# Kernel tuning notes

Hardware: AMD Instinct MI355X
Metric: run time of the kernel (lower is better)

The kernel has to match this reference:

```python
import jax, jax.numpy as jnp
import numpy as np

M, N = 4096, 4096

def _make_expk(n):
    k = np.arange(n, dtype=np.float64) * np.pi / (2.0 * n)
    return jnp.asarray(np.stack([np.cos(k), np.sin(k)], axis=-1), dtype=jnp.float32)

def setup_inputs() -> dict:
    key = jax.random.key(0)
    x = jax.random.normal(key, (M, N), dtype=jnp.float32)
    return {"x": x, "expkM": _make_expk(M), "expkN": _make_expk(N)}

def _idct_last(X, expk):
    """1D IDCT (inverse of unnormalized DCT-II) along last axis via Makhoul's
    N-point FFT trick. expk[k] = (cos, sin) of pi*k/(2N), i.e. e^{j pi k/(2N)}."""
    n = X.shape[-1]
    Xv = X * 0.5
    # V[k] = (Xv[k] - j*Xv[n-k]) * e^{j pi k/(2n)}, with imag part 0 at k=0
    tail = -jnp.flip(Xv, axis=-1)[..., :-1]
    Vi = jnp.concatenate([jnp.zeros_like(Xv[..., :1]), tail], axis=-1)
    W = expk[:, 0] + 1j * expk[:, 1]
    V = (Xv + 1j * Vi) * W
    v = jnp.fft.ifft(V, axis=-1).real.astype(X.dtype)
    # de-interleave: out[2m] = v[m], out[2m+1] = v[n-1-m]
    out = jnp.zeros_like(X)
    out = out.at[..., 0::2].set(v[..., : n - n // 2])
    out = out.at[..., 1::2].set(jnp.flip(v, axis=-1)[..., : n // 2])
    return out

def reference(x, expkM, expkN):
    # separable 2D IDCT: last axis (N) then first axis (M)
    y = _idct_last(x, expkN)
    y = _idct_last(y.T, expkM).T
    return y
```

## Files before the change

### kernel.cpp

```cpp
#include <hip/hip_runtime.h>
#include <math.h>


#define TT 256

constexpr float W64R[32] = {
    1.0f, 0.995184726672197f, 0.980785280403230f, 0.956940335732209f,
    0.923879532511287f, 0.881921264348355f, 0.831469612302545f, 0.773010453362737f,
    0.707106781186548f, 0.634393284163645f, 0.555570233019602f, 0.471396736825998f,
    0.382683432365090f, 0.290284677254462f, 0.195090322016128f, 0.0980171403295606f,
    0.0f, -0.0980171403295606f, -0.195090322016128f, -0.290284677254462f,
    -0.382683432365090f, -0.471396736825998f, -0.555570233019602f, -0.634393284163645f,
    -0.707106781186548f, -0.773010453362737f, -0.831469612302545f, -0.881921264348355f,
    -0.923879532511287f, -0.956940335732209f, -0.980785280403230f, -0.995184726672197f};
constexpr float W64I[32] = {
    0.0f, 0.0980171403295606f, 0.195090322016128f, 0.290284677254462f,
    0.382683432365090f, 0.471396736825998f, 0.555570233019602f, 0.634393284163645f,
    0.707106781186548f, 0.773010453362737f, 0.831469612302545f, 0.881921264348355f,
    0.923879532511287f, 0.956940335732209f, 0.980785280403230f, 0.995184726672197f,
    1.0f, 0.995184726672197f, 0.980785280403230f, 0.956940335732209f,
    0.923879532511287f, 0.881921264348355f, 0.831469612302545f, 0.773010453362737f,
    0.707106781186548f, 0.634393284163645f, 0.555570233019602f, 0.471396736825998f,
    0.382683432365090f, 0.290284677254462f, 0.195090322016128f, 0.0980171403295606f};

__device__ __forceinline__ constexpr int brev(int x, int bits) {
    int r = 0;
    for (int i = 0; i < bits; ++i) { r = (r << 1) | (x & 1); x >>= 1; }
    return r;
}

template <int NP>
__device__ __forceinline__ void fft_dif(float* re, float* im) {
#pragma unroll
    for (int h = NP / 2; h >= 1; h >>= 1) {
#pragma unroll
        for (int b = 0; b < NP; b += 2 * h) {
#pragma unroll
            for (int k = 0; k < h; ++k) {
                float ur = re[b + k], ui = im[b + k];
                float vr = re[b + k + h], vi = im[b + k + h];
                float dr = ur - vr, di = ui - vi;
                re[b + k] = ur + vr;
                im[b + k] = ui + vi;
                float wr = W64R[k * (32 / h)], wi = W64I[k * (32 / h)];
                re[b + k + h] = dr * wr - di * wi;
                im[b + k + h] = dr * wi + di * wr;
            }
        }
    }
}

#define C_SQ2 0.70710678118654752440f
__device__ __forceinline__ void radix8(const float* ar, const float* ai,
                                       float* tr, float* ti) {
    float s04r = ar[0] + ar[4], s04i = ai[0] + ai[4];
    float d04r = ar[0] - ar[4], d04i = ai[0] - ai[4];
    float s26r = ar[2] + ar[6], s26i = ai[2] + ai[6];
    float d26r = ar[2] - ar[6], d26i = ai[2] - ai[6];
    float E0r = s04r + s26r, E0i = s04i + s26i;
    float E1r = d04r - d26i, E1i = d04i + d26r;
    float E2r = s04r - s26r, E2i = s04i - s26i;
    float E3r = d04r + d26i, E3i = d04i - d26r;
    float s15r = ar[1] + ar[5], s15i = ai[1] + ai[5];
    float d15r = ar[1] - ar[5], d15i = ai[1] - ai[5];
    float s37r = ar[3] + ar[7], s37i = ai[3] + ai[7];
    float d37r = ar[3] - ar[7], d37i = ai[3] - ai[7];
    float O0r = s15r + s37r, O0i = s15i + s37i;
    float O1r = d15r - d37i, O1i = d15i + d37r;
    float O2r = s15r - s37r, O2i = s15i - s37i;
    float O3r = d15r + d37i, O3i = d15i - d37r;
    float W1r = C_SQ2 * (O1r - O1i), W1i = C_SQ2 * (O1r + O1i);
    float W2r = -O2i, W2i = O2r;
    float W3r = -C_SQ2 * (O3r + O3i), W3i = C_SQ2 * (O3r - O3i);
    tr[0] = E0r + O0r; ti[0] = E0i + O0i;
    tr[4] = E0r - O0r; ti[4] = E0i - O0i;
    tr[1] = E1r + W1r; ti[1] = E1i + W1i;
    tr[5] = E1r - W1r; ti[5] = E1i - W1i;
    tr[2] = E2r + W2r; ti[2] = E2i + W2i;
    tr[6] = E2r - W2r; ti[6] = E2i - W2i;
    tr[3] = E3r + W3r; ti[3] = E3i + W3i;
    tr[7] = E3r - W3r; ti[7] = E3i - W3i;
}

__global__ __launch_bounds__(TT) void col_a_kernel(
    const float* __restrict__ x, const float4* __restrict__ cAC,
    const float2* __restrict__ tw2048, float2* __restrict__ T1) {
    const int vb = blockIdx.x;
    const int bx = vb & 127, by = vb >> 7;
    const int t = threadIdx.x;
    const int l = t & 63;
    const int ty = t >> 6;
    const int par = l >> 5;
    const int c = bx * 32 + (l & 31);
    const int k1 = by * 4 + ty;
    float fr[16], fi[16];
#pragma unroll
    for (int a = 0; a < 16; ++a) {
        int k = k1 + 64 * (2 * a + par);
        float xa = x[(size_t)k * 4096 + c];
        float xb = x[(size_t)((4096 - k) & 4095) * 4096 + c];
        float xc = x[(size_t)(2048 + k) * 4096 + c];
        float xd = x[(size_t)(2048 - k) * 4096 + c];
        float4 P = cAC[k];
        float bs = (k == 0) ? 0.0f : 1.0f;
        fr[a] = P.x * xa + bs * P.y * xb + P.z * xc + P.w * xd;
        fi[a] = P.y * xa - bs * P.x * xb + P.w * xc - P.z * xd;
    }
    fft_dif<16>(fr, fi);
    const float sgn = par ? -1.0f : 1.0f;
#pragma unroll
    for (int j = 0; j < 16; ++j) {
        int n = brev(j, 4);
        float wr = par ? W64R[2 * n] : 1.0f;
        float wi = par ? W64I[2 * n] : 0.0f;
        float vr = fr[j] * wr - fi[j] * wi;
        float vi = fr[j] * wi + fi[j] * wr;
        float orr = __shfl_xor(vr, 32, 64);
        float oii = __shfl_xor(vi, 32, 64);
        float zr = orr + sgn * vr;
        float zi = oii + sgn * vi;
        int n2 = par ? (n + 16) : n;
        float2 w2 = tw2048[k1 * n2];
        float2 o = make_float2(zr * w2.x - zi * w2.y,
                               zr * w2.y + zi * w2.x);
        T1[(size_t)(n2 * 64 + k1) * 4096 + c] = o;
    }
}

__global__ __launch_bounds__(TT, 1) void col_b_kernel(
    const float2* __restrict__ T1, float* __restrict__ out) {
    const int vb = blockIdx.x;
    const int bx = vb & 127, by = vb >> 7;
    const int t = threadIdx.x;
    const int wv = t >> 6;
    const int l = t & 63;
    const int par = l >> 5;
    const int c = bx * 32 + (l & 31);
    const int n2 = by * 4 + wv;
    float fr[32], fi[32];
#pragma unroll
    for (int a = 0; a < 32; ++a) {
        int k1 = 2 * a + par;
        float2 v = T1[(size_t)(n2 * 64 + k1) * 4096 + c];
        fr[a] = v.x; fi[a] = v.y;
    }
    fft_dif<32>(fr, fi);
    const float sgn = par ? -1.0f : 1.0f;
#pragma unroll
    for (int j = 0; j < 32; ++j) {
        int n = brev(j, 5);
        float wr = par ? W64R[n] : 1.0f;
        float wi = par ? W64I[n] : 0.0f;
        float vr = fr[j] * wr - fi[j] * wi;
        float vi = fr[j] * wi + fi[j] * wr;
        float orr = __shfl_xor(vr, 32, 64);
        float oii = __shfl_xor(vi, 32, 64);
        float zr = orr + sgn * vr;
        float zi = oii + sgn * vi;
        int n1 = par ? (n + 32) : n;
        int m = 32 * n1 + n2;
        int r_re = (n1 < 32) ? 4 * m     : 8191 - 4 * m;
        int r_im = (n1 < 32) ? 4 * m + 2 : 8189 - 4 * m;
        out[(size_t)r_re * 4096 + c] = zr;
        out[(size_t)r_im * 4096 + c] = zi;
    }
}

__global__ __launch_bounds__(TT) void idct_rows_kernel(
    const float2* __restrict__ ca, const float2* __restrict__ cb,
    const float2* __restrict__ cc, const float2* __restrict__ cd,
    const float2* __restrict__ tw2048, float* __restrict__ io) {
    __shared__ float pool[8576];
    float* b0r = pool;
    float* b0i = pool + 2112;
    float* b1r = pool + 4224;
    float* b1i = pool + 6400;
    float* stg = pool + 4224;
    const int t = threadIdx.x;
    float* __restrict__ xr = io + (size_t)blockIdx.x * 4096;

#pragma unroll
    for (int u = 0; u < 4; ++u) {
        int idx = t + 256 * u;
        float4 v = ((const float4*)xr)[idx];
        *(float4*)&stg[4 * idx] = v;
    }
    __syncthreads();

    float zr[8], zi[8], tr[8], ti[8];
#pragma unroll
    for (int p = 0; p < 8; ++p) {
        int k = t + 256 * p;
        float xa = stg[k];
        float xb = stg[(4096 - k) & 4095];
        float xc = stg[2048 + k];
        float xd = stg[2048 - k];
        float2 A = ca[k], B = cb[k], C = cc[k], D = cd[k];
        zr[p] = A.x * xa + B.x * xb + C.x * xc + D.x * xd;
        zi[p] = A.y * xa + B.y * xb + C.y * xc + D.y * xd;
    }
    radix8(zr, zi, tr, ti);
    {
        int baseA = 8 * t + (t >> 2);
        b0r[baseA] = tr[0]; b0i[baseA] = ti[0];
#pragma unroll
        for (int q = 1; q < 8; ++q) {
            float2 w = tw2048[(t * q) & 2047];
            b0r[baseA + q] = w.x * tr[q] - w.y * ti[q];
            b0i[baseA + q] = w.x * ti[q] + w.y * tr[q];
        }
    }
    __syncthreads();
    {
        float ar[8], ai[8];
        int rb = t + (t >> 5);
#pragma unroll
        for (int p = 0; p < 8; ++p) { ar[p] = b0r[rb + 264 * p]; ai[p] = b0i[rb + 264 * p]; }
        radix8(ar, ai, tr, ti);
        int j = t >> 3, k = t & 7, wj = 8 * j;
        int baseB = 68 * j + k;
        b1r[baseB] = tr[0]; b1i[baseB] = ti[0];
#pragma unroll
        for (int q = 1; q < 8; ++q) {
            int off = baseB + 8 * q + (q >> 1);
            float2 w = tw2048[(wj * q) & 2047];
            b1r[off] = w.x * tr[q] - w.y * ti[q];
            b1i[off] = w.x * ti[q] + w.y * tr[q];
        }
    }
    __syncthreads();
    {
        float ar[8], ai[8];
        int rb = t + (t >> 4);
#pragma unroll
        for (int p = 0; p < 8; ++p) { ar[p] = b1r[rb + 272 * p]; ai[p] = b1i[rb + 272 * p]; }
        radix8(ar, ai, tr, ti);
        int j = t >> 6, wj = 64 * j, k = t & 63;
        int baseC = 528 * j + k + (k >> 5);
        b0r[baseC] = tr[0]; b0i[baseC] = ti[0];
#pragma unroll
        for (int q = 1; q < 8; ++q) {
            int off = baseC + 66 * q;
            float2 w = tw2048[(wj * q) & 2047];
            b0r[off] = w.x * tr[q] - w.y * ti[q];
            b0i[off] = w.x * ti[q] + w.y * tr[q];
        }
    }
    __syncthreads();
#pragma unroll
    for (int u = 0; u < 2; ++u) {
        int b = t + 256 * u;
        int rb = b + (b >> 5);
        int wb = b + (b >> 4);
        float a0r = b0r[rb], a0i = b0i[rb];
        float a1r = b0r[rb + 528], a1i = b0i[rb + 528];
        float a2r = b0r[rb + 1056], a2i = b0i[rb + 1056];
        float a3r = b0r[rb + 1584], a3i = b0i[rb + 1584];
        float s02r = a0r + a2r, s02i = a0i + a2i;
        float d02r = a0r - a2r, d02i = a0i - a2i;
        float s13r = a1r + a3r, s13i = a1i + a3i;
        float d13r = a1r - a3r, d13i = a1i - a3i;
        b1r[wb] = s02r + s13r;          b1i[wb] = s02i + s13i;
        b1r[wb + 544] = d02r - d13i;    b1i[wb + 544] = d02i + d13r;
        b1r[wb + 1088] = s02r - s13r;   b1i[wb + 1088] = s02i - s13i;
        b1r[wb + 1632] = d02r + d13i;   b1i[wb + 1632] = d02i - d13r;
    }
    __syncthreads();
#pragma unroll
    for (int i = 0; i < 4; ++i) {
        int s = t + 256 * i;
        int l2 = 2047 - s;
        int ms = s + (s >> 4);
        int ml = l2 + (l2 >> 4);
        float4 o = make_float4(b1r[ms], b1i[ml], b1i[ms], b1r[ml]);
        *(float4*)&xr[4 * s] = o;
    }
}

#define TABLE_BYTES (7 * 16384)
static void build_tables_host(char* blob) {
    float2* tw2048 = (float2*)blob;
    float2* ca = (float2*)(blob + 1 * 16384);
    float2* cb = (float2*)(blob + 2 * 16384);
    float2* cc = (float2*)(blob + 3 * 16384);
    float2* cd = (float2*)(blob + 4 * 16384);
    float4* cAC = (float4*)(blob + 5 * 16384);
    const double s = 0.5 / 4096.0;
    for (int k = 0; k < 2048; ++k) {
        double aw = M_PI * (double)k / 2048.0;
        double wr = cos(aw), wi = sin(aw);
        double a1 = M_PI * (double)k / 8192.0;
        double e1r = cos(a1), e1i = sin(a1);
        double a2 = M_PI * (double)(k + 2048) / 8192.0;
        double e2r = cos(a2), e2i = sin(a2);
        double Ar = s * ((1.0 - wi) * e1r - wr * e1i);
        double Ai = s * ((1.0 - wi) * e1i + wr * e1r);
        double Br = (k == 0) ? 0.0 : Ai;
        double Bi = (k == 0) ? 0.0 : -Ar;
        double Cr = s * ((1.0 + wi) * e2r + wr * e2i);
        double Ci = s * ((1.0 + wi) * e2i - wr * e2r);
        ca[k] = make_float2((float)Ar, (float)Ai);
        cb[k] = make_float2((float)Br, (float)Bi);
        cc[k] = make_float2((float)Cr, (float)Ci);
        cd[k] = make_float2((float)Ci, (float)-Cr);
        cAC[k] = make_float4((float)Ar, (float)Ai, (float)Cr, (float)Ci);
        double at = M_PI * (double)k / 1024.0;
        tw2048[k] = make_float2((float)cos(at), (float)sin(at));
    }
}

extern "C" void kernel_launch(void* const* d_in, const int* in_sizes, int n_in,
                              void* d_out, int out_size, void* d_ws, size_t ws_size,
                              hipStream_t stream) {
    const float* x = (const float*)d_in[0];
    float* out = (float*)d_out;

    float2* tw2048 = (float2*)d_ws;
    float2* ca = (float2*)((char*)d_ws + 1 * 16384);
    float2* cb = (float2*)((char*)d_ws + 2 * 16384);
    float2* cc = (float2*)((char*)d_ws + 3 * 16384);
    float2* cd = (float2*)((char*)d_ws + 4 * 16384);
    float4* cAC = (float4*)((char*)d_ws + 5 * 16384);
    float2* T1 = (float2*)((char*)d_ws + (1 << 20));

    static char* h_tables = nullptr;
    if (!h_tables) {
        h_tables = new char[TABLE_BYTES];
        build_tables_host(h_tables);
    }
    hipMemcpyAsync(d_ws, h_tables, TABLE_BYTES, hipMemcpyHostToDevice, stream);

    col_a_kernel<<<2048, TT, 0, stream>>>(x, cAC, tw2048, T1);
    col_b_kernel<<<1024, TT, 0, stream>>>(T1, out);
    idct_rows_kernel<<<4096, TT, 0, stream>>>(ca, cb, cc, cd, tw2048, out);
}
```

Before: 209.4 us.

## Generate twiddle tables on device and compute col_a twiddles inline

Removes the per-call host-to-device copy of precomputed twiddle tables. The first blocks of col_a now build the tables used by the row kernel in double precision. col_a itself computes its coefficients and twiddles on the fly with hardware sin/cos instead of loading them from tables. This trades memory traffic and a memcpy for transcendental ALU work and possible float accuracy loss; the approximate hardware sin/cos on larger arguments may reduce precision.

```diff
diff --git a/kernel.cpp b/kernel.cpp
--- a/kernel.cpp
+++ b/kernel.cpp
@@ -83,16 +83,44 @@
 }
 
 __global__ __launch_bounds__(TT) void col_a_kernel(
-    const float* __restrict__ x, const float4* __restrict__ cAC,
-    const float2* __restrict__ tw2048, float2* __restrict__ T1) {
+    const float* __restrict__ x,
+    float2* __restrict__ tw2048,
+    float2* __restrict__ ca, float2* __restrict__ cb,
+    float2* __restrict__ cc, float2* __restrict__ cd,
+    float2* __restrict__ T1) {
     const int vb = blockIdx.x;
+    const int t = threadIdx.x;
+
+    if (vb < 8) {
+        int k = vb * TT + t;
+        const double s = 0.5 / 4096.0;
+        double aw = M_PI * (double)k / 2048.0;
+        double wr = cos(aw), wi = sin(aw);
+        double a1 = M_PI * (double)k / 8192.0;
+        double e1r = cos(a1), e1i = sin(a1);
+        double a2 = M_PI * (double)(k + 2048) / 8192.0;
+        double e2r = cos(a2), e2i = sin(a2);
+        double Ar = s * ((1.0 - wi) * e1r - wr * e1i);
+        double Ai = s * ((1.0 - wi) * e1i + wr * e1r);
+        double Br = (k == 0) ? 0.0 : Ai;
+        double Bi = (k == 0) ? 0.0 : -Ar;
+        double Cr = s * ((1.0 + wi) * e2r + wr * e2i);
+        double Ci = s * ((1.0 + wi) * e2i - wr * e2r);
+        ca[k] = make_float2((float)Ar, (float)Ai);
+        cb[k] = make_float2((float)Br, (float)Bi);
+        cc[k] = make_float2((float)Cr, (float)Ci);
+        cd[k] = make_float2((float)Ci, (float)-Cr);
+        double at = M_PI * (double)k / 1024.0;
+        tw2048[k] = make_float2((float)cos(at), (float)sin(at));
+    }
+
     const int bx = vb & 127, by = vb >> 7;
-    const int t = threadIdx.x;
     const int l = t & 63;
     const int ty = t >> 6;
     const int par = l >> 5;
     const int c = bx * 32 + (l & 31);
     const int k1 = by * 4 + ty;
+    const float S = 0.5f / 4096.0f;
     float fr[16], fi[16];
 #pragma unroll
     for (int a = 0; a < 16; ++a) {
@@ -101,10 +129,22 @@
         float xb = x[(size_t)((4096 - k) & 4095) * 4096 + c];
         float xc = x[(size_t)(2048 + k) * 4096 + c];
         float xd = x[(size_t)(2048 - k) * 4096 + c];
-        float4 P = cAC[k];
+        float rw = (float)k * (1.0f / 4096.0f);
+        float wr = __builtin_amdgcn_cosf(rw);
+        float wi = __builtin_amdgcn_sinf(rw);
+        float r1 = (float)k * (1.0f / 16384.0f);
+        float e1r = __builtin_amdgcn_cosf(r1);
+        float e1i = __builtin_amdgcn_sinf(r1);
+        float e2r = C_SQ2 * (e1r - e1i);
+        float e2i = C_SQ2 * (e1r + e1i);
+        float omw = 1.0f - wi, opw = 1.0f + wi;
+        float Ar = S * (omw * e1r - wr * e1i);
+        float Ai = S * (omw * e1i + wr * e1r);
+        float Cr = S * (opw * e2r + wr * e2i);
+        float Ci = S * (opw * e2i - wr * e2r);
         float bs = (k == 0) ? 0.0f : 1.0f;
-        fr[a] = P.x * xa + bs * P.y * xb + P.z * xc + P.w * xd;
-        fi[a] = P.y * xa - bs * P.x * xb + P.w * xc - P.z * xd;
+        fr[a] = Ar * xa + bs * Ai * xb + Cr * xc + Ci * xd;
+        fi[a] = Ai * xa - bs * Ar * xb + Ci * xc - Cr * xd;
     }
     fft_dif<16>(fr, fi);
     const float sgn = par ? -1.0f : 1.0f;
@@ -120,9 +160,11 @@
         float zr = orr + sgn * vr;
         float zi = oii + sgn * vi;
         int n2 = par ? (n + 16) : n;
-        float2 w2 = tw2048[k1 * n2];
-        float2 o = make_float2(zr * w2.x - zi * w2.y,
-                               zr * w2.y + zi * w2.x);
+        float rv = (float)(k1 * n2) * (1.0f / 2048.0f);
+        float twr = __builtin_amdgcn_cosf(rv);
+        float twi = __builtin_amdgcn_sinf(rv);
+        float2 o = make_float2(zr * twr - zi * twi,
+                               zr * twi + zi * twr);
         T1[(size_t)(n2 * 64 + k1) * 4096 + c] = o;
     }
 }
@@ -277,38 +319,6 @@
     }
 }
 
-#define TABLE_BYTES (7 * 16384)
-static void build_tables_host(char* blob) {
-    float2* tw2048 = (float2*)blob;
-    float2* ca = (float2*)(blob + 1 * 16384);
-    float2* cb = (float2*)(blob + 2 * 16384);
-    float2* cc = (float2*)(blob + 3 * 16384);
-    float2* cd = (float2*)(blob + 4 * 16384);
-    float4* cAC = (float4*)(blob + 5 * 16384);
-    const double s = 0.5 / 4096.0;
-    for (int k = 0; k < 2048; ++k) {
-        double aw = M_PI * (double)k / 2048.0;
-        double wr = cos(aw), wi = sin(aw);
-        double a1 = M_PI * (double)k / 8192.0;
-        double e1r = cos(a1), e1i = sin(a1);
-        double a2 = M_PI * (double)(k + 2048) / 8192.0;
-        double e2r = cos(a2), e2i = sin(a2);
-        double Ar = s * ((1.0 - wi) * e1r - wr * e1i);
-        double Ai = s * ((1.0 - wi) * e1i + wr * e1r);
-        double Br = (k == 0) ? 0.0 : Ai;
-        double Bi = (k == 0) ? 0.0 : -Ar;
-        double Cr = s * ((1.0 + wi) * e2r + wr * e2i);
-        double Ci = s * ((1.0 + wi) * e2i - wr * e2r);
-        ca[k] = make_float2((float)Ar, (float)Ai);
-        cb[k] = make_float2((float)Br, (float)Bi);
-        cc[k] = make_float2((float)Cr, (float)Ci);
-        cd[k] = make_float2((float)Ci, (float)-Cr);
-        cAC[k] = make_float4((float)Ar, (float)Ai, (float)Cr, (float)Ci);
-        double at = M_PI * (double)k / 1024.0;
-        tw2048[k] = make_float2((float)cos(at), (float)sin(at));
-    }
-}
-
 extern "C" void kernel_launch(void* const* d_in, const int* in_sizes, int n_in,
                               void* d_out, int out_size, void* d_ws, size_t ws_size,
                               hipStream_t stream) {
@@ -320,17 +330,9 @@
     float2* cb = (float2*)((char*)d_ws + 2 * 16384);
     float2* cc = (float2*)((char*)d_ws + 3 * 16384);
     float2* cd = (float2*)((char*)d_ws + 4 * 16384);
-    float4* cAC = (float4*)((char*)d_ws + 5 * 16384);
     float2* T1 = (float2*)((char*)d_ws + (1 << 20));
 
-    static char* h_tables = nullptr;
-    if (!h_tables) {
-        h_tables = new char[TABLE_BYTES];
-        build_tables_host(h_tables);
-    }
-    hipMemcpyAsync(d_ws, h_tables, TABLE_BYTES, hipMemcpyHostToDevice, stream);
-
-    col_a_kernel<<<2048, TT, 0, stream>>>(x, cAC, tw2048, T1);
+    col_a_kernel<<<2048, TT, 0, stream>>>(x, tw2048, ca, cb, cc, cd, T1);
     col_b_kernel<<<1024, TT, 0, stream>>>(T1, out);
     idct_rows_kernel<<<4096, TT, 0, stream>>>(ca, cb, cc, cd, tw2048, out);
 }
```

Result: faster. 187.4 us (-10.5%).
